# Kernel optimization log

Measured on AMD Instinct MI355X. Metric: run time of the kernel, lower is better.

The kernel has to match this reference:

```python
import jax, jax.numpy as jnp
import numpy as np

N, E, D_IN, D_H, D_OUT, W = 100000, 1600000, 128, 128, 128, 3
HTC_W, TEMP = 0.01, 1.0  # curvature c = 1.0


def _project(x):
    n = jnp.maximum(jnp.linalg.norm(x, axis=-1, keepdims=True), 1e-12)
    return x * jnp.minimum((1.0 - 1e-5) / n, 1.0)


def _artanh(x):
    x = jnp.clip(x, -1.0 + 1e-6, 1.0 - 1e-6)
    return 0.5 * (jnp.log1p(x) - jnp.log1p(-x))


def _expmap0(v):
    n = jnp.maximum(jnp.linalg.norm(v, axis=-1, keepdims=True), 1e-12)
    return _project(jnp.tanh(n) * v / n)


def _logmap0(y):
    y = _project(y)
    n = jnp.maximum(jnp.linalg.norm(y, axis=-1, keepdims=True), 1e-12)
    return _artanh(n) * y / n


def setup_inputs() -> dict:
    key = jax.random.key(0)
    ks = jax.random.split(key, 24)
    x = jax.random.normal(ks[0], (N, D_IN), dtype=jnp.float32)
    edge_index = jax.random.randint(ks[1], (2, E), 0, N)
    t = jax.random.uniform(ks[2], (E,), dtype=jnp.float32)
    prev_hyp = _project(jax.random.normal(ks[3], (N, D_OUT), dtype=jnp.float32) * 0.05)
    lengths = jax.random.randint(ks[4], (N,), 0, W + 1)
    valid_mask = jnp.arange(W)[None, :] < lengths[:, None]  # front-filled deque
    hist_hyp = _project(jax.random.normal(ks[5], (N, W, D_OUT), dtype=jnp.float32) * 0.05)
    hist_hyp = hist_hyp * valid_mask[..., None].astype(jnp.float32)  # padded slots are zero

    def lin(k, dout, din):
        return jax.random.normal(k, (dout, din), dtype=jnp.float32) / np.sqrt(din)

    params = dict(
        w_time=jax.random.normal(ks[6], (D_IN,), dtype=jnp.float32),
        b_time=jnp.zeros((D_IN,), jnp.float32),
        W0_l=lin(ks[7], D_H, D_IN), b0_l=jnp.zeros((D_H,), jnp.float32), W0_r=lin(ks[8], D_H, D_IN),
        W1_l=lin(ks[9], D_OUT, D_H), b1_l=jnp.zeros((D_OUT,), jnp.float32), W1_r=lin(ks[10], D_OUT, D_H),
        W_ih=lin(ks[11], 3 * D_OUT, D_OUT), W_hh=lin(ks[12], 3 * D_OUT, D_OUT),
        b_ih=jnp.zeros((3 * D_OUT,), jnp.float32), b_hh=jnp.zeros((3 * D_OUT,), jnp.float32),
        Wq=lin(ks[13], D_OUT, D_OUT), Wk=lin(ks[14], D_OUT, D_OUT), Wv=lin(ks[15], D_OUT, D_OUT),
    )
    return dict(x=x, edge_index=edge_index, t=t, prev_hyp=prev_hyp,
                hist_hyp=hist_hyp, valid_mask=valid_mask, **params)


def reference(x, edge_index, t, prev_hyp, hist_hyp, valid_mask,
              w_time, b_time, W0_l, b0_l, W0_r, W1_l, b1_l, W1_r,
              W_ih, W_hh, b_ih, b_hh, Wq, Wk, Wv):
    n = x.shape[0]
    src, dst = edge_index[0], edge_index[1]
    ones_e = jnp.ones_like(t)
    # per-node mean event time over incident edges (src and dst both count)
    nt = jax.ops.segment_sum(t, src, n) + jax.ops.segment_sum(t, dst, n)
    cnt = jax.ops.segment_sum(ones_e, src, n) + jax.ops.segment_sum(ones_e, dst, n)
    node_time = nt / jnp.maximum(cnt, 1.0)
    x = x + jnp.cos(node_time[:, None] * w_time[None, :] + b_time[None, :])
    # SAGEConv (mean aggr over incoming edges): out = W_l @ mean_j x_j + b + W_r @ x_i
    deg = jnp.maximum(jax.ops.segment_sum(ones_e, dst, n), 1.0)[:, None]
    agg0 = jax.ops.segment_sum(x[src], dst, n) / deg
    h = jax.nn.relu(agg0 @ W0_l.T + b0_l + x @ W0_r.T)
    agg1 = jax.ops.segment_sum(h[src], dst, n) / deg
    h_now = agg1 @ W1_l.T + b1_l + h @ W1_r.T  # tangent-space current embedding

    prev_tan = _logmap0(prev_hyp)
    # ragged history attention (padded + masked)
    hist_tan = _logmap0(hist_hyp)                       # [N, W, D]
    q = h_now @ Wq.T                                    # [N, D]
    k = hist_tan @ Wk.T                                 # [N, W, D]
    v = hist_tan @ Wv.T
    score = jnp.einsum('nwd,nd->nw', k, q) / (np.sqrt(D_OUT) * max(TEMP, 1e-6))
    has_hist = valid_mask.any(axis=-1, keepdims=True)
    score = jnp.where(valid_mask, score, -jnp.inf)
    score = jnp.where(has_hist, score, 0.0)
    alpha = jax.nn.softmax(score, axis=-1)
    alpha = jnp.where(has_hist, alpha, 0.0)
    ctx = jnp.einsum('nw,nwd->nd', alpha, v)

    # GRUCell(input=h_now, hidden=prev_tan + ctx)
    hidden = prev_tan + ctx
    gi = h_now @ W_ih.T + b_ih
    gh = hidden @ W_hh.T + b_hh
    i_r, i_z, i_n = jnp.split(gi, 3, axis=-1)
    h_r, h_z, h_n = jnp.split(gh, 3, axis=-1)
    r = jax.nn.sigmoid(i_r + h_r)
    z = jax.nn.sigmoid(i_z + h_z)
    nn_ = jnp.tanh(i_n + r * h_n)
    h_tan = (1.0 - z) * nn_ + z * hidden
    h_hyp = _expmap0(h_tan)

    # hyperbolic temporal consistency aux loss (c = 1)
    x_sq = jnp.sum(h_hyp * h_hyp, axis=-1)
    y_sq = jnp.sum(prev_hyp * prev_hyp, axis=-1)
    diff_sq = jnp.sum((h_hyp - prev_hyp) ** 2, axis=-1)
    denom = jnp.maximum((1.0 - x_sq) * (1.0 - y_sq), 1e-8)
    zarg = jnp.maximum(1.0 + 2.0 * diff_sq / denom, 1.0 + 1e-6)
    dist = jnp.arccosh(zarg)
    valid_prev = (jnp.sum(jnp.abs(prev_hyp), axis=-1) > 0).astype(dist.dtype)
    aux = HTC_W * jnp.sum(dist * valid_prev) / jnp.maximum(jnp.sum(valid_prev), 1.0)
    aux = jnp.where(jnp.any(valid_prev > 0), aux, 0.0)
    return h_hyp, aux
```

## Files before the change

kernel.cpp:

```cpp
#include <hip/hip_runtime.h>
#include <math.h>


typedef _Float16 f16x8 __attribute__((ext_vector_type(8)));
typedef _Float16 f16x4 __attribute__((ext_vector_type(4)));
typedef _Float16 f16x2 __attribute__((ext_vector_type(2)));
typedef float f32x4 __attribute__((ext_vector_type(4)));

__device__ __forceinline__ float wsum(float v) {
#pragma unroll
  for (int off = 1; off < 64; off <<= 1) v += __shfl_xor(v, off, 64);
  return v;
}

__device__ __forceinline__ void fsplit(float x, _Float16& h, _Float16& l) {
  h = (_Float16)x;
  l = (_Float16)(x - (float)h);
}

__device__ __forceinline__ float logmap_scale(float nrm2) {
  float n0 = fmaxf(sqrtf(nrm2), 1e-12f);
  float sp = fminf((1.0f - 1e-5f) / n0, 1.0f);
  float np = fmaxf(n0 * sp, 1e-12f);
  float a  = fminf(np, 1.0f - 1e-6f);
  float at = 0.5f * (log1pf(a) - log1pf(-a));
  return sp * at / np;
}

__global__ void k_edge(const int* __restrict__ ei, const float* __restrict__ t,
                       unsigned long long* __restrict__ packed, int E) {
  int e = blockIdx.x * 256 + threadIdx.x;
  if (e >= E) return;
  int s = ei[e], d = ei[E + e];
  unsigned long long tf =
      (unsigned long long)__float2uint_rn(t[e] * 16777216.0f);
  unsigned long long encs = tf | (1ULL << 40);
  atomicAdd(&packed[s], encs);
  atomicAdd(&packed[d], encs | (1ULL << 52));
}

__global__ void k_scan1(const unsigned long long* __restrict__ packed,
                        int* __restrict__ rowptr, int* __restrict__ bsum, int N) {
  __shared__ int s[256];
  int t = threadIdx.x;
  int base = blockIdx.x * 1024 + t * 4;
  int v[4]; int loc = 0;
#pragma unroll
  for (int j = 0; j < 4; ++j) {
    int i = base + j;
    v[j] = (i < N) ? (int)(packed[i] >> 52) : 0;
    loc += v[j];
  }
  s[t] = loc; __syncthreads();
  for (int off = 1; off < 256; off <<= 1) {
    int x = (t >= off) ? s[t - off] : 0; __syncthreads();
    s[t] += x; __syncthreads();
  }
  int run = s[t] - loc;
#pragma unroll
  for (int j = 0; j < 4; ++j) { int i = base + j; if (i < N) rowptr[i] = run; run += v[j]; }
  if (t == 255) bsum[blockIdx.x] = s[255];
}

__global__ void k_scan2(const int* __restrict__ bsum, int* __restrict__ boff, int nb) {
  __shared__ int s[128];
  int t = threadIdx.x;
  int v = (t < nb) ? bsum[t] : 0;
  s[t] = v; __syncthreads();
  for (int off = 1; off < 128; off <<= 1) {
    int x = (t >= off) ? s[t - off] : 0; __syncthreads();
    s[t] += x; __syncthreads();
  }
  boff[t] = s[t] - v;
}

__global__ void k_scan3(int* __restrict__ rowptr, const int* __restrict__ boff, int N, int E) {
  int i = blockIdx.x * 256 + threadIdx.x;
  if (i < N) rowptr[i] += boff[i >> 10];
  if (i == 0) rowptr[N] = E;
}

__global__ void k_scatter(const int* __restrict__ ei, const int* __restrict__ rowptr,
                          int* __restrict__ cursor, int* __restrict__ eidx, int E) {
  int e = blockIdx.x * 256 + threadIdx.x;
  if (e >= E) return;
  int s = ei[e], d = ei[E + e];
  int p = rowptr[d] + atomicAdd(&cursor[d], 1);
  eidx[p] = s;
}

__global__ void k_time(const float* __restrict__ x,
                       const unsigned long long* __restrict__ packed,
                       const float* __restrict__ wt,
                       const float* __restrict__ bt,
                       _Float16* __restrict__ out, int N) {
  int id = blockIdx.x * 256 + threadIdx.x;
  if (id >= N * 32) return;
  int n = id >> 5, q = id & 31;
  unsigned long long p = packed[n];
  float tsum = (float)(p & 0xFFFFFFFFFFULL) * 5.9604644775390625e-8f;
  int c = (int)((p >> 40) & 0xFFF);
  float tm = tsum / fmaxf((float)c, 1.0f);
  float4 xv = ((const float4*)x)[id];
  float4 wv = ((const float4*)wt)[q];
  float4 bv = ((const float4*)bt)[q];
  float o[4];
  o[0] = xv.x + cosf(tm * wv.x + bv.x);
  o[1] = xv.y + cosf(tm * wv.y + bv.y);
  o[2] = xv.z + cosf(tm * wv.z + bv.z);
  o[3] = xv.w + cosf(tm * wv.w + bv.w);
  f16x4 vh, vl;
#pragma unroll
  for (int j = 0; j < 4; ++j) { _Float16 h, l; fsplit(o[j], h, l); vh[j] = h; vl[j] = l; }
  *(f16x4*)&out[(size_t)n * 256 + q * 4] = vh;
  *(f16x4*)&out[(size_t)n * 256 + 128 + q * 4] = vl;
}

__global__ void k_agg(const _Float16* __restrict__ X, const int* __restrict__ rowptr,
                      const int* __restrict__ eidx, _Float16* __restrict__ out, int N) {
  int wid = threadIdx.x >> 6, lane = threadIdx.x & 63;
  int n = blockIdx.x * 4 + wid;
  if (n >= N) return;
  int s0 = rowptr[n], s1 = rowptr[n + 1];
  size_t lo4 = (size_t)lane * 4;
  float a0[4] = {0, 0, 0, 0}, a1[4] = {0, 0, 0, 0};
  float a2[4] = {0, 0, 0, 0}, a3[4] = {0, 0, 0, 0};
  int e = s0;
  for (; e + 4 <= s1; e += 4) {
    int i0 = eidx[e], i1 = eidx[e + 1], i2 = eidx[e + 2], i3 = eidx[e + 3];
    f16x4 v0 = *(const f16x4*)&X[(size_t)i0 * 256 + lo4];
    f16x4 v1 = *(const f16x4*)&X[(size_t)i1 * 256 + lo4];
    f16x4 v2 = *(const f16x4*)&X[(size_t)i2 * 256 + lo4];
    f16x4 v3 = *(const f16x4*)&X[(size_t)i3 * 256 + lo4];
#pragma unroll
    for (int j = 0; j < 4; ++j) {
      a0[j] += (float)v0[j]; a1[j] += (float)v1[j];
      a2[j] += (float)v2[j]; a3[j] += (float)v3[j];
    }
  }
  float a[4];
#pragma unroll
  for (int j = 0; j < 4; ++j) a[j] = (a0[j] + a1[j]) + (a2[j] + a3[j]);
  for (; e < s1; ++e) {
    int s = eidx[e];
    f16x4 v = *(const f16x4*)&X[(size_t)s * 256 + lo4];
#pragma unroll
    for (int j = 0; j < 4; ++j) a[j] += (float)v[j];
  }
  float lov[4];
#pragma unroll
  for (int j = 0; j < 4; ++j) lov[j] = __shfl(a[j], lane + 32, 64);
  if (lane < 32) {
    float sc = 1.0f / fmaxf((float)(s1 - s0), 1.0f);
    f16x4 vh, vl;
#pragma unroll
    for (int j = 0; j < 4; ++j) {
      float v = (a[j] + lov[j]) * sc;
      _Float16 h, l; fsplit(v, h, l);
      vh[j] = h; vl[j] = l;
    }
    *(f16x4*)&out[(size_t)n * 256 + lane * 4] = vh;
    *(f16x4*)&out[(size_t)n * 256 + 128 + lane * 4] = vl;
  }
}

__global__ void k_prep(const float* __restrict__ W0l, const float* __restrict__ W0r,
                       const float* __restrict__ W1l, const float* __restrict__ W1r,
                       const float* __restrict__ Wv,  const float* __restrict__ Wih,
                       const float* __restrict__ Whh, const float* __restrict__ bih,
                       const float* __restrict__ bhh,
                       _Float16* __restrict__ W0H, _Float16* __restrict__ W0L,
                       _Float16* __restrict__ W1H, _Float16* __restrict__ W1L,
                       _Float16* __restrict__ WvH, _Float16* __restrict__ WvL,
                       _Float16* __restrict__ WzH, _Float16* __restrict__ WzL,
                       float* __restrict__ bz) {
  int id = blockIdx.x * 256 + threadIdx.x;
  if (id < 32768) {
    int c = id >> 8, k = id & 255;
    float v0 = (k < 128) ? W0l[c * 128 + k] : W0r[c * 128 + (k - 128)];
    float v1 = (k < 128) ? W1l[c * 128 + k] : W1r[c * 128 + (k - 128)];
    fsplit(v0, W0H[id], W0L[id]);
    fsplit(v1, W1H[id], W1L[id]);
  }
  if (id < 16384) {
    fsplit(Wv[id], WvH[id], WvL[id]);
  }
  if (id < 131072) {
    int c = id >> 8, k = id & 255;
    float v;
    if (c < 256)      v = (k < 128) ? Wih[c * 128 + k] : Whh[c * 128 + (k - 128)];
    else if (c < 384) v = (k < 128) ? Wih[c * 128 + k] : 0.f;
    else              v = (k < 128) ? 0.f : Whh[(c - 128) * 128 + (k - 128)];
    fsplit(v, WzH[id], WzL[id]);
  }
  if (id < 512) {
    float v;
    if (id < 256)      v = bih[id] + bhh[id];
    else if (id < 384) v = bih[id];
    else               v = bhh[id - 128];
    bz[id] = v;
  }
}

__global__ void k_ct(const float* __restrict__ Wk, const float* __restrict__ Wq,
                     _Float16* __restrict__ CtH, _Float16* __restrict__ CtL) {
  int id = blockIdx.x * 256 + threadIdx.x;
  if (id >= 16384) return;
  int c = id >> 7, k = id & 127;
  float s = 0.f;
  for (int j = 0; j < 128; ++j) s += Wk[j * 128 + c] * Wq[j * 128 + k];
  fsplit(s, CtH[id], CtL[id]);
}

__global__ void k_lognorm(const float* __restrict__ Y, float* __restrict__ scale, int N) {
  int wid = threadIdx.x >> 6, lane = threadIdx.x & 63;
  int n = blockIdx.x * 4 + wid;
  if (n >= N) return;
  float2 y = ((const float2*)Y)[(size_t)n * 64 + lane];
  float nrm2 = wsum(y.x * y.x + y.y * y.y);
  if (lane == 0) scale[n] = logmap_scale(nrm2);
}

__global__ __launch_bounds__(256)
void k_mm(const _Float16* __restrict__ A1, const _Float16* __restrict__ A2,
          const _Float16* __restrict__ WH,  const _Float16* __restrict__ WL,
          const float* __restrict__ bias,   const float* __restrict__ addb,
          const float* __restrict__ scalev,
          float* __restrict__ outF, _Float16* __restrict__ outS,
          int Nrows, int Ktot, int Ctot, int relu) {
  __shared__ _Float16 sA[2][128][64];
  __shared__ _Float16 sW[2][128][64];
  const int tid = threadIdx.x;
  const int lane = tid & 63;
  const int wv = tid >> 6;
  const int wr = wv >> 1, wc = wv & 1;
  const int laneR = lane & 15, laneG = lane >> 4;
  const int n0 = blockIdx.x * 128;
  const int c0 = blockIdx.y * 128;

  f32x4 acc[4][4];
#pragma unroll
  for (int mi = 0; mi < 4; ++mi)
#pragma unroll
    for (int ni = 0; ni < 4; ++ni)
#pragma unroll
      for (int j = 0; j < 4; ++j) acc[mi][ni][j] = 0.f;

  const int nslab = Ktot >> 6;
  for (int s = 0; s < nslab; ++s) {
    int kglob = s << 6;
    const _Float16* Ax = (kglob < 128) ? A1 : A2;
    int kc = kglob & 127;
    __syncthreads();
#pragma unroll
    for (int it = 0; it < 4; ++it) {
      int idx = tid + (it << 8);
      int r = idx >> 3, chunk = idx & 7;
      int cs = (chunk ^ (r & 7)) << 3;
      int kq = chunk << 3;
      int n = n0 + r;
      f16x8 vh, vl;
      if (n < Nrows) {
        vh = *(const f16x8*)&Ax[(size_t)n * 256 + kc + kq];
        vl = *(const f16x8*)&Ax[(size_t)n * 256 + 128 + kc + kq];
      } else {
#pragma unroll
        for (int j = 0; j < 8; ++j) { vh[j] = (_Float16)0; vl[j] = (_Float16)0; }
      }
      *(f16x8*)&sA[0][r][cs] = vh;
      *(f16x8*)&sA[1][r][cs] = vl;
      int c = c0 + r;
      f16x8 wh = *(const f16x8*)&WH[(size_t)c * Ktot + kglob + kq];
      f16x8 wl = *(const f16x8*)&WL[(size_t)c * Ktot + kglob + kq];
      *(f16x8*)&sW[0][r][cs] = wh;
      *(f16x8*)&sW[1][r][cs] = wl;
    }
    __syncthreads();
#pragma unroll
    for (int kk = 0; kk < 2; ++kk) {
      f16x8 ah[4], al[4], bh[4], bl[4];
      int kch = (kk << 2) + laneG;
#pragma unroll
      for (int m = 0; m < 4; ++m) {
        int row = wr * 64 + m * 16 + laneR;
        int ko = (kch ^ (row & 7)) << 3;
        ah[m] = *(const f16x8*)&sA[0][row][ko];
        al[m] = *(const f16x8*)&sA[1][row][ko];
      }
#pragma unroll
      for (int n = 0; n < 4; ++n) {
        int row = wc * 64 + n * 16 + laneR;
        int ko = (kch ^ (row & 7)) << 3;
        bh[n] = *(const f16x8*)&sW[0][row][ko];
        bl[n] = *(const f16x8*)&sW[1][row][ko];
      }
#pragma unroll
      for (int m = 0; m < 4; ++m)
#pragma unroll
        for (int n = 0; n < 4; ++n) {
          acc[m][n] = __builtin_amdgcn_mfma_f32_16x16x32_f16(ah[m], bh[n], acc[m][n], 0, 0, 0);
          acc[m][n] = __builtin_amdgcn_mfma_f32_16x16x32_f16(al[m], bh[n], acc[m][n], 0, 0, 0);
          acc[m][n] = __builtin_amdgcn_mfma_f32_16x16x32_f16(ah[m], bl[n], acc[m][n], 0, 0, 0);
        }
    }
  }
#pragma unroll
  for (int m = 0; m < 4; ++m) {
#pragma unroll
    for (int n = 0; n < 4; ++n) {
      int rbase = n0 + wr * 64 + m * 16 + laneG * 4;
      int c = c0 + wc * 64 + n * 16 + laneR;
      float bval = bias ? bias[c] : 0.f;
#pragma unroll
      for (int j = 0; j < 4; ++j) {
        int r = rbase + j;
        if (r >= Nrows) continue;
        float v = acc[m][n][j] + bval;
        if (addb) {
          float ab = addb[(size_t)r * Ctot + c];
          v += scalev ? ab * scalev[r] : ab;
        }
        if (relu) v = fmaxf(v, 0.f);
        if (outF) outF[(size_t)r * Ctot + c] = v;
        if (outS) {
          _Float16 h, l; fsplit(v, h, l);
          outS[(size_t)r * 256 + c] = h;
          outS[(size_t)r * 256 + 128 + c] = l;
        }
      }
    }
  }
}

__global__ __launch_bounds__(256)
void k_mmu(const _Float16* __restrict__ A1, const _Float16* __restrict__ A2,
           const _Float16* __restrict__ WH, const _Float16* __restrict__ WL,
           const _Float16* __restrict__ CtH, const _Float16* __restrict__ CtL,
           const float* __restrict__ bias,
           _Float16* __restrict__ outS, float* __restrict__ outU, int Nrows) {
  __shared__ _Float16 sA[2][128][64];
  __shared__ _Float16 sW[2][128][64];
  const int tid = threadIdx.x;
  const int lane = tid & 63;
  const int wv = tid >> 6;
  const int wr = wv >> 1, wc = wv & 1;
  const int laneR = lane & 15, laneG = lane >> 4;
  const int n0 = blockIdx.x * 128;

  f32x4 acc[4][4];
#pragma unroll
  for (int mi = 0; mi < 4; ++mi)
#pragma unroll
    for (int ni = 0; ni < 4; ++ni)
#pragma unroll
      for (int j = 0; j < 4; ++j) acc[mi][ni][j] = 0.f;

  for (int s = 0; s < 4; ++s) {
    int kglob = s << 6;
    const _Float16* Ax = (kglob < 128) ? A1 : A2;
    int kc = kglob & 127;
    __syncthreads();
#pragma unroll
    for (int it = 0; it < 4; ++it) {
      int idx = tid + (it << 8);
      int r = idx >> 3, chunk = idx & 7;
      int cs = (chunk ^ (r & 7)) << 3;
      int kq = chunk << 3;
      int n = n0 + r;
      f16x8 vh, vl;
      if (n < Nrows) {
        vh = *(const f16x8*)&Ax[(size_t)n * 256 + kc + kq];
        vl = *(const f16x8*)&Ax[(size_t)n * 256 + 128 + kc + kq];
      } else {
#pragma unroll
        for (int j = 0; j < 8; ++j) { vh[j] = (_Float16)0; vl[j] = (_Float16)0; }
      }
      *(f16x8*)&sA[0][r][cs] = vh;
      *(f16x8*)&sA[1][r][cs] = vl;
      f16x8 wh = *(const f16x8*)&WH[(size_t)r * 256 + kglob + kq];
      f16x8 wl = *(const f16x8*)&WL[(size_t)r * 256 + kglob + kq];
      *(f16x8*)&sW[0][r][cs] = wh;
      *(f16x8*)&sW[1][r][cs] = wl;
    }
    __syncthreads();
#pragma unroll
    for (int kk = 0; kk < 2; ++kk) {
      f16x8 ah[4], al[4], bh[4], bl[4];
      int kch = (kk << 2) + laneG;
#pragma unroll
      for (int m = 0; m < 4; ++m) {
        int row = wr * 64 + m * 16 + laneR;
        int ko = (kch ^ (row & 7)) << 3;
        ah[m] = *(const f16x8*)&sA[0][row][ko];
        al[m] = *(const f16x8*)&sA[1][row][ko];
      }
#pragma unroll
      for (int n = 0; n < 4; ++n) {
        int row = wc * 64 + n * 16 + laneR;
        int ko = (kch ^ (row & 7)) << 3;
        bh[n] = *(const f16x8*)&sW[0][row][ko];
        bl[n] = *(const f16x8*)&sW[1][row][ko];
      }
#pragma unroll
      for (int m = 0; m < 4; ++m)
#pragma unroll
        for (int n = 0; n < 4; ++n) {
          acc[m][n] = __builtin_amdgcn_mfma_f32_16x16x32_f16(ah[m], bh[n], acc[m][n], 0, 0, 0);
          acc[m][n] = __builtin_amdgcn_mfma_f32_16x16x32_f16(al[m], bh[n], acc[m][n], 0, 0, 0);
          acc[m][n] = __builtin_amdgcn_mfma_f32_16x16x32_f16(ah[m], bl[n], acc[m][n], 0, 0, 0);
        }
    }
  }

  f32x4 accU[4][4];
#pragma unroll
  for (int mi = 0; mi < 4; ++mi)
#pragma unroll
    for (int ni = 0; ni < 4; ++ni)
#pragma unroll
      for (int j = 0; j < 4; ++j) accU[mi][ni][j] = 0.f;

  for (int us = 0; us < 2; ++us) {
    __syncthreads();
    if (wc == us) {
#pragma unroll
      for (int m = 0; m < 4; ++m)
#pragma unroll
        for (int n = 0; n < 4; ++n) {
          int kp = n * 16 + laneR;
          float bval = bias[us * 64 + n * 16 + laneR];
#pragma unroll
          for (int j = 0; j < 4; ++j) {
            int row = wr * 64 + m * 16 + laneG * 4 + j;
            float v = acc[m][n][j] + bval;
            _Float16 h, l; fsplit(v, h, l);
            int cs = ((kp >> 3) ^ (row & 7)) * 8 + (kp & 7);
            sA[0][row][cs] = h;
            sA[1][row][cs] = l;
          }
        }
    }
#pragma unroll
    for (int it = 0; it < 4; ++it) {
      int idx = tid + (it << 8);
      int r = idx >> 3, chunk = idx & 7;
      int cs = (chunk ^ (r & 7)) << 3;
      int kq = chunk << 3;
      *(f16x8*)&sW[0][r][cs] = *(const f16x8*)&CtH[(size_t)r * 128 + us * 64 + kq];
      *(f16x8*)&sW[1][r][cs] = *(const f16x8*)&CtL[(size_t)r * 128 + us * 64 + kq];
    }
    __syncthreads();
#pragma unroll
    for (int kk = 0; kk < 2; ++kk) {
      f16x8 ah[4], al[4], bh[4], bl[4];
      int kch = (kk << 2) + laneG;
#pragma unroll
      for (int m = 0; m < 4; ++m) {
        int row = wr * 64 + m * 16 + laneR;
        int ko = (kch ^ (row & 7)) << 3;
        ah[m] = *(const f16x8*)&sA[0][row][ko];
        al[m] = *(const f16x8*)&sA[1][row][ko];
      }
#pragma unroll
      for (int n = 0; n < 4; ++n) {
        int row = wc * 64 + n * 16 + laneR;
        int ko = (kch ^ (row & 7)) << 3;
        bh[n] = *(const f16x8*)&sW[0][row][ko];
        bl[n] = *(const f16x8*)&sW[1][row][ko];
      }
#pragma unroll
      for (int m = 0; m < 4; ++m)
#pragma unroll
        for (int n = 0; n < 4; ++n) {
          accU[m][n] = __builtin_amdgcn_mfma_f32_16x16x32_f16(ah[m], bh[n], accU[m][n], 0, 0, 0);
          accU[m][n] = __builtin_amdgcn_mfma_f32_16x16x32_f16(al[m], bh[n], accU[m][n], 0, 0, 0);
          accU[m][n] = __builtin_amdgcn_mfma_f32_16x16x32_f16(ah[m], bl[n], accU[m][n], 0, 0, 0);
        }
    }
  }

#pragma unroll
  for (int m = 0; m < 4; ++m) {
#pragma unroll
    for (int n = 0; n < 4; ++n) {
      int rbase = n0 + wr * 64 + m * 16 + laneG * 4;
      int c = wc * 64 + n * 16 + laneR;
      float bval = bias[c];
#pragma unroll
      for (int j = 0; j < 4; ++j) {
        int r = rbase + j;
        if (r >= Nrows) continue;
        float v = acc[m][n][j] + bval;
        _Float16 h, l; fsplit(v, h, l);
        outS[(size_t)r * 256 + c] = h;
        outS[(size_t)r * 256 + 128 + c] = l;
        outU[(size_t)r * 128 + c] = accU[m][n][j];
      }
    }
  }
}

__global__ void k_attn(const float* __restrict__ U, const float* __restrict__ hist,
                       _Float16* __restrict__ out, int N) {
  int wid = threadIdx.x >> 6, lane = threadIdx.x & 63;
  int n = blockIdx.x * 4 + wid;
  if (n >= N) return;
  float2 u = ((const float2*)U)[(size_t)n * 64 + lane];
  float htx[3], hty[3], sc[3];
  bool val[3];
#pragma unroll
  for (int w = 0; w < 3; ++w) {
    float2 h = ((const float2*)hist)[((size_t)n * 3 + w) * 64 + lane];
    float nrm2 = wsum(h.x * h.x + h.y * h.y);
    val[w] = nrm2 > 0.f;
    float s = logmap_scale(nrm2);
    htx[w] = h.x * s; hty[w] = h.y * s;
    float d = wsum(htx[w] * u.x + hty[w] * u.y);
    sc[w] = d * 0.0883883476483184f;
  }
  float cx = 0.f, cy = 0.f;
  if (val[0] || val[1] || val[2]) {
    float m = -INFINITY;
#pragma unroll
    for (int w = 0; w < 3; ++w) if (val[w]) m = fmaxf(m, sc[w]);
    float a[3]; float ssum = 0.f;
#pragma unroll
    for (int w = 0; w < 3; ++w) { a[w] = val[w] ? expf(sc[w] - m) : 0.f; ssum += a[w]; }
    float inv = 1.f / ssum;
#pragma unroll
    for (int w = 0; w < 3; ++w) { cx += htx[w] * (a[w] * inv); cy += hty[w] * (a[w] * inv); }
  }
  _Float16 hx, lx, hy, ly;
  fsplit(cx, hx, lx); fsplit(cy, hy, ly);
  f16x2 vh = {hx, hy}, vl = {lx, ly};
  *(f16x2*)&out[(size_t)n * 256 + lane * 2] = vh;
  *(f16x2*)&out[(size_t)n * 256 + 128 + lane * 2] = vl;
}

__global__ __launch_bounds__(256, 2)
void k_gru(const _Float16* __restrict__ P0c, const _Float16* __restrict__ P2c,
           const _Float16* __restrict__ WzH, const _Float16* __restrict__ WzL,
           const float* __restrict__ bz, const float* __restrict__ prev,
           float* __restrict__ out, float* __restrict__ pd,
           float* __restrict__ pv, int N) {
  __shared__ _Float16 sA[2][64][64];
  __shared__ _Float16 sW[2][128][64];
  __shared__ float rn1[64][2];
  __shared__ float rn3[64][2][3];
  __shared__ float distrow[64], validrow[64];
  const int tid = threadIdx.x;
  const int lane = tid & 63;
  const int wv = tid >> 6;
  const int wr = wv >> 1, wc = wv & 1;
  const int laneR = lane & 15, laneG = lane >> 4;
  const int n0 = blockIdx.x * 64;

  f32x4 acc[4][2][4];
#pragma unroll
  for (int q = 0; q < 4; ++q)
#pragma unroll
    for (int m = 0; m < 2; ++m)
#pragma unroll
      for (int n = 0; n < 4; ++n)
#pragma unroll
        for (int j = 0; j < 4; ++j) acc[q][m][n][j] = 0.f;

#define STAGE_W(Q)                                                          \
  {                                                                         \
    _Pragma("unroll")                                                       \
    for (int it = 0; it < 4; ++it) {                                        \
      int idx = tid + (it << 8);                                            \
      int r = idx >> 3, chunk = idx & 7;                                    \
      int cs = (chunk ^ (r & 7)) << 3;                                      \
      int kq = chunk << 3;                                                  \
      size_t wrow = (size_t)((Q)*128 + r);                                  \
      *(f16x8*)&sW[0][r][cs] = *(const f16x8*)&WzH[wrow * 256 + kglob + kq];\
      *(f16x8*)&sW[1][r][cs] = *(const f16x8*)&WzL[wrow * 256 + kglob + kq];\
    }                                                                       \
  }

#define COMPUTE_Q(Q)                                                        \
  {                                                                         \
    _Pragma("unroll")                                                       \
    for (int kk = 0; kk < 2; ++kk) {                                        \
      int kch = (kk << 2) + laneG;                                          \
      f16x8 ah[2], al[2], bh[4], bl[4];                                     \
      _Pragma("unroll")                                                     \
      for (int m = 0; m < 2; ++m) {                                         \
        int row = wr * 32 + m * 16 + laneR;                                 \
        int ko = (kch ^ (row & 7)) << 3;                                    \
        ah[m] = *(const f16x8*)&sA[0][row][ko];                             \
        al[m] = *(const f16x8*)&sA[1][row][ko];                             \
      }                                                                     \
      _Pragma("unroll")                                                     \
      for (int n = 0; n < 4; ++n) {                                         \
        int row = wc * 64 + n * 16 + laneR;                                 \
        int ko = (kch ^ (row & 7)) << 3;                                    \
        bh[n] = *(const f16x8*)&sW[0][row][ko];                             \
        bl[n] = *(const f16x8*)&sW[1][row][ko];                             \
      }                                                                     \
      _Pragma("unroll")                                                     \
      for (int m = 0; m < 2; ++m)                                           \
        _Pragma("unroll")                                                   \
        for (int n = 0; n < 4; ++n) {                                       \
          acc[Q][m][n] = __builtin_amdgcn_mfma_f32_16x16x32_f16(ah[m], bh[n], acc[Q][m][n], 0, 0, 0); \
          acc[Q][m][n] = __builtin_amdgcn_mfma_f32_16x16x32_f16(al[m], bh[n], acc[Q][m][n], 0, 0, 0); \
          acc[Q][m][n] = __builtin_amdgcn_mfma_f32_16x16x32_f16(ah[m], bl[n], acc[Q][m][n], 0, 0, 0); \
        }                                                                   \
    }                                                                       \
  }

#pragma unroll
  for (int s = 0; s < 4; ++s) {
    int kglob = s << 6;
    const _Float16* Ax = (s < 2) ? P0c : P2c;
    int kc = kglob & 127;
    __syncthreads();
#pragma unroll
    for (int it = 0; it < 2; ++it) {
      int idx = tid + (it << 8);
      int r = idx >> 3, chunk = idx & 7;
      int cs = (chunk ^ (r & 7)) << 3;
      int kq = chunk << 3;
      int n = n0 + r;
      f16x8 vh, vl;
      if (n < N) {
        vh = *(const f16x8*)&Ax[(size_t)n * 256 + kc + kq];
        vl = *(const f16x8*)&Ax[(size_t)n * 256 + 128 + kc + kq];
      } else {
#pragma unroll
        for (int j = 0; j < 8; ++j) { vh[j] = (_Float16)0; vl[j] = (_Float16)0; }
      }
      *(f16x8*)&sA[0][r][cs] = vh;
      *(f16x8*)&sA[1][r][cs] = vl;
    }
    STAGE_W(0);
    __syncthreads();
    COMPUTE_Q(0);
    __syncthreads();
    STAGE_W(1);
    __syncthreads();
    COMPUTE_Q(1);
    __syncthreads();
    if (s < 2) {
      STAGE_W(2);
      __syncthreads();
      COMPUTE_Q(2);
    } else {
      STAGE_W(3);
      __syncthreads();
      COMPUTE_Q(3);
    }
  }
#undef STAGE_W
#undef COMPUTE_Q

  float bz0[4], bz1[4], bz2[4], bz3[4];
#pragma unroll
  for (int n = 0; n < 4; ++n) {
    int d = wc * 64 + n * 16 + laneR;
    bz0[n] = bz[d]; bz1[n] = bz[128 + d]; bz2[n] = bz[256 + d]; bz3[n] = bz[384 + d];
  }
  float tv[2][4][4];
#pragma unroll
  for (int m = 0; m < 2; ++m)
#pragma unroll
    for (int n = 0; n < 4; ++n)
#pragma unroll
      for (int j = 0; j < 4; ++j) {
        int row = n0 + wr * 32 + m * 16 + laneG * 4 + j;
        int d = wc * 64 + n * 16 + laneR;
        float hid = 0.f;
        if (row < N) {
          size_t o = (size_t)row * 256 + d;
          hid = (float)P2c[o] + (float)P2c[o + 128];
        }
        float gr = acc[0][m][n][j] + bz0[n];
        float gz = acc[1][m][n][j] + bz1[n];
        float gi = acc[2][m][n][j] + bz2[n];
        float gh = acc[3][m][n][j] + bz3[n];
        float rr = 1.f / (1.f + expf(-gr));
        float zz = 1.f / (1.f + expf(-gz));
        float nn = tanhf(gi + rr * gh);
        tv[m][n][j] = (1.f - zz) * nn + zz * hid;
      }
#pragma unroll
  for (int m = 0; m < 2; ++m)
#pragma unroll
    for (int j = 0; j < 4; ++j) {
      float p = 0.f;
#pragma unroll
      for (int n = 0; n < 4; ++n) p += tv[m][n][j] * tv[m][n][j];
#pragma unroll
      for (int off = 1; off < 16; off <<= 1) p += __shfl_xor(p, off, 64);
      if (laneR == 0) rn1[wr * 32 + m * 16 + laneG * 4 + j][wc] = p;
    }
  __syncthreads();
  float hv[2][4][4];
#pragma unroll
  for (int m = 0; m < 2; ++m)
#pragma unroll
    for (int j = 0; j < 4; ++j) {
      int rl = wr * 32 + m * 16 + laneG * 4 + j;
      int row = n0 + rl;
      float nv2 = rn1[rl][0] + rn1[rl][1];
      float nv = fmaxf(sqrtf(nv2), 1e-12f);
      float tn = tanhf(nv);
      float s1 = tn / nv;
      float nw = fmaxf(tn, 1e-12f);
      float sp = fminf((1.f - 1e-5f) / nw, 1.f);
      float scl = s1 * sp;
#pragma unroll
      for (int n = 0; n < 4; ++n) {
        float h = tv[m][n][j] * scl;
        hv[m][n][j] = h;
        int d = wc * 64 + n * 16 + laneR;
        if (row < N) out[(size_t)row * 128 + d] = h;
      }
    }
#pragma unroll
  for (int m = 0; m < 2; ++m)
#pragma unroll
    for (int j = 0; j < 4; ++j) {
      int rl = wr * 32 + m * 16 + laneG * 4 + j;
      int row = n0 + rl;
      float ys = 0.f, ds = 0.f, pa = 0.f;
#pragma unroll
      for (int n = 0; n < 4; ++n) {
        int d = wc * 64 + n * 16 + laneR;
        float p = (row < N) ? prev[(size_t)row * 128 + d] : 0.f;
        float h = hv[m][n][j];
        ys += p * p; ds += (h - p) * (h - p); pa += fabsf(p);
      }
#pragma unroll
      for (int off = 1; off < 16; off <<= 1) {
        ys += __shfl_xor(ys, off, 64);
        ds += __shfl_xor(ds, off, 64);
        pa += __shfl_xor(pa, off, 64);
      }
      if (laneR == 0) { rn3[rl][wc][0] = ys; rn3[rl][wc][1] = ds; rn3[rl][wc][2] = pa; }
    }
  __syncthreads();
  if (wc == 0 && laneR == 0) {
#pragma unroll
    for (int m = 0; m < 2; ++m)
#pragma unroll
      for (int j = 0; j < 4; ++j) {
        int rl = wr * 32 + m * 16 + laneG * 4 + j;
        int row = n0 + rl;
        float nv2 = rn1[rl][0] + rn1[rl][1];
        float nv = fmaxf(sqrtf(nv2), 1e-12f);
        float tn = tanhf(nv);
        float s1 = tn / nv;
        float nw = fmaxf(tn, 1e-12f);
        float sp = fminf((1.f - 1e-5f) / nw, 1.f);
        float scl = s1 * sp;
        float x_sq = scl * scl * nv2;
        float y_sq = rn3[rl][0][0] + rn3[rl][1][0];
        float d_sq = rn3[rl][0][1] + rn3[rl][1][1];
        float pab  = rn3[rl][0][2] + rn3[rl][1][2];
        float denom = fmaxf((1.f - x_sq) * (1.f - y_sq), 1e-8f);
        float zarg = fmaxf(1.f + 2.f * d_sq / denom, 1.f + 1e-6f);
        float dist = acoshf(zarg);
        float valid = (pab > 0.f && row < N) ? 1.f : 0.f;
        distrow[rl] = dist * valid;
        validrow[rl] = valid;
      }
  }
  __syncthreads();
  if (tid < 64) {
    float dv = distrow[tid], vvv = validrow[tid];
    dv = wsum(dv); vvv = wsum(vvv);
    if (tid == 0) { pd[blockIdx.x] = dv; pv[blockIdx.x] = vvv; }
  }
}

__global__ void k_reduce(const float* __restrict__ pd, const float* __restrict__ pv,
                         float* __restrict__ aux_out, int nparts) {
  __shared__ float sd[256], sv[256];
  float a = 0.f, b = 0.f;
  for (int i = threadIdx.x; i < nparts; i += 256) { a += pd[i]; b += pv[i]; }
  sd[threadIdx.x] = a; sv[threadIdx.x] = b; __syncthreads();
  for (int off = 128; off > 0; off >>= 1) {
    if (threadIdx.x < off) { sd[threadIdx.x] += sd[threadIdx.x + off]; sv[threadIdx.x] += sv[threadIdx.x + off]; }
    __syncthreads();
  }
  if (threadIdx.x == 0) {
    float aux = (sv[0] > 0.f) ? 0.01f * sd[0] / fmaxf(sv[0], 1.f) : 0.f;
    aux_out[0] = aux;
  }
}

extern "C" void kernel_launch(void* const* d_in, const int* in_sizes, int n_in,
                              void* d_out, int out_size, void* d_ws, size_t ws_size,
                              hipStream_t stream) {
  const float* x      = (const float*)d_in[0];
  const int*   ei     = (const int*)  d_in[1];
  const float* t      = (const float*)d_in[2];
  const float* prev   = (const float*)d_in[3];
  const float* hist   = (const float*)d_in[4];
  const float* w_time = (const float*)d_in[6];
  const float* b_time = (const float*)d_in[7];
  const float* W0l    = (const float*)d_in[8];
  const float* b0l    = (const float*)d_in[9];
  const float* W0r    = (const float*)d_in[10];
  const float* W1l    = (const float*)d_in[11];
  const float* b1l    = (const float*)d_in[12];
  const float* W1r    = (const float*)d_in[13];
  const float* Wih    = (const float*)d_in[14];
  const float* Whh    = (const float*)d_in[15];
  const float* bih    = (const float*)d_in[16];
  const float* bhh    = (const float*)d_in[17];
  const float* Wq     = (const float*)d_in[18];
  const float* Wk     = (const float*)d_in[19];
  const float* Wv     = (const float*)d_in[20];

  const int N = in_sizes[0] / 128;
  const int E = in_sizes[1] / 2;
  const int NB4 = (N + 3) / 4;
  const int NB1 = (N + 1023) / 1024;
  const int NBG = (N + 63) / 64;

  char* wbase = (char*)d_ws;
  size_t off = 0;
  auto alloc = [&](size_t bytes) -> void* {
    off = (off + 255) & ~(size_t)255;
    void* p = wbase + off; off += bytes; return p;
  };
  unsigned long long* packed = (unsigned long long*)alloc((size_t)N * 8);
  int*   cursor = (int*)  alloc((size_t)N * 4);
  size_t zero_bytes = off;
  int*   rowptr = (int*)  alloc((size_t)(N + 1) * 4);
  int*   bsum   = (int*)  alloc(512);
  int*   boff   = (int*)  alloc(512);
  int*   eidx   = (int*)  alloc((size_t)E * 4);
  _Float16* W0H = (_Float16*)alloc(32768 * 2);
  _Float16* W0L = (_Float16*)alloc(32768 * 2);
  _Float16* W1H = (_Float16*)alloc(32768 * 2);
  _Float16* W1L = (_Float16*)alloc(32768 * 2);
  _Float16* CtH = (_Float16*)alloc(16384 * 2);
  _Float16* CtL = (_Float16*)alloc(16384 * 2);
  _Float16* WvH = (_Float16*)alloc(16384 * 2);
  _Float16* WvL = (_Float16*)alloc(16384 * 2);
  _Float16* WzH = (_Float16*)alloc(131072 * 2);
  _Float16* WzL = (_Float16*)alloc(131072 * 2);
  float* bz     = (float*)alloc(512 * 4);
  float* scale  = (float*)alloc((size_t)N * 4);
  float* F0     = (float*)alloc((size_t)N * 128 * 4);
  _Float16* P0c = (_Float16*)alloc((size_t)N * 256 * 2);
  _Float16* P1c = (_Float16*)alloc((size_t)N * 256 * 2);
  _Float16* P2c = (_Float16*)alloc((size_t)N * 256 * 2);
  float* pd = (float*)alloc((size_t)NBG * 4);
  float* pv = (float*)alloc((size_t)NBG * 4);
  (void)ws_size; (void)n_in; (void)out_size;

  float* out_h   = (float*)d_out;
  float* out_aux = out_h + (size_t)N * 128;

  hipMemsetAsync(d_ws, 0, zero_bytes, stream);

  k_prep<<<512, 256, 0, stream>>>(W0l, W0r, W1l, W1r, Wv, Wih, Whh, bih, bhh,
                                  W0H, W0L, W1H, W1L, WvH, WvL, WzH, WzL, bz);
  k_ct<<<64, 256, 0, stream>>>(Wk, Wq, CtH, CtL);
  k_lognorm<<<NB4, 256, 0, stream>>>(prev, scale, N);

  int ebl = (E + 255) / 256;
  k_edge<<<ebl, 256, 0, stream>>>(ei, t, packed, E);
  k_scan1<<<NB1, 256, 0, stream>>>(packed, rowptr, bsum, N);
  k_scan2<<<1, 128, 0, stream>>>(bsum, boff, NB1);
  k_scan3<<<(N + 255) / 256, 256, 0, stream>>>(rowptr, boff, N, E);
  k_scatter<<<ebl, 256, 0, stream>>>(ei, rowptr, cursor, eidx, E);

  k_time<<<(N * 32 + 255) / 256, 256, 0, stream>>>(x, packed, w_time, b_time,
                                                   P0c, N);
  k_agg<<<NB4, 256, 0, stream>>>(P0c, rowptr, eidx, P1c, N);
  dim3 gb((N + 127) / 128, 1);
  k_mm<<<gb, 256, 0, stream>>>(P1c, P0c, W0H, W0L, b0l, nullptr, nullptr,
                               nullptr, P2c, N, 256, 128, 1);
  k_agg<<<NB4, 256, 0, stream>>>(P2c, rowptr, eidx, P1c, N);
  k_mmu<<<gb, 256, 0, stream>>>(P1c, P2c, W1H, W1L, CtH, CtL, b1l, P0c, F0, N);
  k_attn<<<NB4, 256, 0, stream>>>(F0, hist, P1c, N);
  k_mm<<<gb, 256, 0, stream>>>(P1c, nullptr, WvH, WvL, nullptr, prev, scale,
                               nullptr, P2c, N, 128, 128, 0);
  k_gru<<<NBG, 256, 0, stream>>>(P0c, P2c, WzH, WzL, bz, prev,
                                 out_h, pd, pv, N);
  k_reduce<<<1, 256, 0, stream>>>(pd, pv, out_aux, NBG);
}
```

Measured before the change: 1.122 ms.

## Merge independent prep kernels and load GEMM tiles directly into LDS

Independent setup kernels (edge atomics, weight splitting, Ct product, log-norm scale) are merged into one launch through block-range dispatch, and scatter is merged with the time-encoding kernel, cutting launch count and letting the pieces overlap. The GEMM tile loads in k_mm and k_mmu switch from global-to-register-to-LDS copies to global_load_lds direct transfers with a per-lane XOR-swizzled source address. Out-of-range rows are clamped to the last valid row instead of being zero-filled, which is only safe if those rows are never written back. The direct-to-LDS layout relies on the wave-contiguous write order matching the swizzled read pattern.

```diff
diff --git a/kernel.cpp b/kernel.cpp
--- a/kernel.cpp
+++ b/kernel.cpp
@@ -16,6 +16,12 @@
 __device__ __forceinline__ void fsplit(float x, _Float16& h, _Float16& l) {
   h = (_Float16)x;
   l = (_Float16)(x - (float)h);
+}
+
+typedef const __attribute__((address_space(1))) unsigned int* gas_ptr;
+typedef __attribute__((address_space(3))) unsigned int* las_ptr;
+__device__ __forceinline__ void gld16(const void* g, void* l) {
+  __builtin_amdgcn_global_load_lds((gas_ptr)g, (las_ptr)l, 16, 0, 0);
 }
 
 __device__ __forceinline__ float logmap_scale(float nrm2) {
@@ -27,16 +33,82 @@
   return sp * at / np;
 }
 
-__global__ void k_edge(const int* __restrict__ ei, const float* __restrict__ t,
-                       unsigned long long* __restrict__ packed, int E) {
-  int e = blockIdx.x * 256 + threadIdx.x;
-  if (e >= E) return;
-  int s = ei[e], d = ei[E + e];
-  unsigned long long tf =
-      (unsigned long long)__float2uint_rn(t[e] * 16777216.0f);
-  unsigned long long encs = tf | (1ULL << 40);
-  atomicAdd(&packed[s], encs);
-  atomicAdd(&packed[d], encs | (1ULL << 52));
+__global__ void k_edgeprep(const int* __restrict__ ei, const float* __restrict__ t,
+                           unsigned long long* __restrict__ packed, int E, int ebl,
+                           const float* __restrict__ Wk, const float* __restrict__ Wq,
+                           _Float16* __restrict__ CtH, _Float16* __restrict__ CtL,
+                           const float* __restrict__ prevY, float* __restrict__ scale,
+                           int N, int NB4,
+                           const float* __restrict__ W0l, const float* __restrict__ W0r,
+                           const float* __restrict__ W1l, const float* __restrict__ W1r,
+                           const float* __restrict__ Wv,  const float* __restrict__ Wih,
+                           const float* __restrict__ Whh, const float* __restrict__ bih,
+                           const float* __restrict__ bhh,
+                           _Float16* __restrict__ W0H, _Float16* __restrict__ W0L,
+                           _Float16* __restrict__ W1H, _Float16* __restrict__ W1L,
+                           _Float16* __restrict__ WvH, _Float16* __restrict__ WvL,
+                           _Float16* __restrict__ WzH, _Float16* __restrict__ WzL,
+                           float* __restrict__ bz) {
+  int bid = blockIdx.x;
+  if (bid < ebl) {
+    int e = bid * 256 + threadIdx.x;
+    if (e >= E) return;
+    int s = ei[e], d = ei[E + e];
+    unsigned long long tf =
+        (unsigned long long)__float2uint_rn(t[e] * 16777216.0f);
+    unsigned long long encs = tf | (1ULL << 40);
+    atomicAdd(&packed[s], encs);
+    atomicAdd(&packed[d], encs | (1ULL << 52));
+    return;
+  }
+  bid -= ebl;
+  if (bid < 64) {
+    int id = bid * 256 + threadIdx.x;
+    int c = id >> 7, k = id & 127;
+    float s = 0.f;
+    for (int j = 0; j < 128; ++j) s += Wk[j * 128 + c] * Wq[j * 128 + k];
+    fsplit(s, CtH[id], CtL[id]);
+    return;
+  }
+  bid -= 64;
+  if (bid < NB4) {
+    int wid = threadIdx.x >> 6, lane = threadIdx.x & 63;
+    int n = bid * 4 + wid;
+    if (n >= N) return;
+    float2 y = ((const float2*)prevY)[(size_t)n * 64 + lane];
+    float nrm2 = wsum(y.x * y.x + y.y * y.y);
+    if (lane == 0) scale[n] = logmap_scale(nrm2);
+    return;
+  }
+  bid -= NB4;
+  {
+    int id = bid * 256 + threadIdx.x;
+    if (id < 32768) {
+      int c = id >> 8, k = id & 255;
+      float v0 = (k < 128) ? W0l[c * 128 + k] : W0r[c * 128 + (k - 128)];
+      float v1 = (k < 128) ? W1l[c * 128 + k] : W1r[c * 128 + (k - 128)];
+      fsplit(v0, W0H[id], W0L[id]);
+      fsplit(v1, W1H[id], W1L[id]);
+    }
+    if (id < 16384) {
+      fsplit(Wv[id], WvH[id], WvL[id]);
+    }
+    if (id < 131072) {
+      int c = id >> 8, k = id & 255;
+      float v;
+      if (c < 256)      v = (k < 128) ? Wih[c * 128 + k] : Whh[c * 128 + (k - 128)];
+      else if (c < 384) v = (k < 128) ? Wih[c * 128 + k] : 0.f;
+      else              v = (k < 128) ? 0.f : Whh[(c - 128) * 128 + (k - 128)];
+      fsplit(v, WzH[id], WzL[id]);
+    }
+    if (id < 512) {
+      float v;
+      if (id < 256)      v = bih[id] + bhh[id];
+      else if (id < 384) v = bih[id];
+      else               v = bhh[id - 128];
+      bz[id] = v;
+    }
+  }
 }
 
 __global__ void k_scan1(const unsigned long long* __restrict__ packed,
@@ -80,40 +152,45 @@
   if (i == 0) rowptr[N] = E;
 }
 
-__global__ void k_scatter(const int* __restrict__ ei, const int* __restrict__ rowptr,
-                          int* __restrict__ cursor, int* __restrict__ eidx, int E) {
-  int e = blockIdx.x * 256 + threadIdx.x;
-  if (e >= E) return;
-  int s = ei[e], d = ei[E + e];
-  int p = rowptr[d] + atomicAdd(&cursor[d], 1);
-  eidx[p] = s;
-}
-
-__global__ void k_time(const float* __restrict__ x,
-                       const unsigned long long* __restrict__ packed,
-                       const float* __restrict__ wt,
-                       const float* __restrict__ bt,
-                       _Float16* __restrict__ out, int N) {
-  int id = blockIdx.x * 256 + threadIdx.x;
-  if (id >= N * 32) return;
-  int n = id >> 5, q = id & 31;
-  unsigned long long p = packed[n];
-  float tsum = (float)(p & 0xFFFFFFFFFFULL) * 5.9604644775390625e-8f;
-  int c = (int)((p >> 40) & 0xFFF);
-  float tm = tsum / fmaxf((float)c, 1.0f);
-  float4 xv = ((const float4*)x)[id];
-  float4 wv = ((const float4*)wt)[q];
-  float4 bv = ((const float4*)bt)[q];
-  float o[4];
-  o[0] = xv.x + cosf(tm * wv.x + bv.x);
-  o[1] = xv.y + cosf(tm * wv.y + bv.y);
-  o[2] = xv.z + cosf(tm * wv.z + bv.z);
-  o[3] = xv.w + cosf(tm * wv.w + bv.w);
-  f16x4 vh, vl;
-#pragma unroll
-  for (int j = 0; j < 4; ++j) { _Float16 h, l; fsplit(o[j], h, l); vh[j] = h; vl[j] = l; }
-  *(f16x4*)&out[(size_t)n * 256 + q * 4] = vh;
-  *(f16x4*)&out[(size_t)n * 256 + 128 + q * 4] = vl;
+__global__ void k_scattime(const int* __restrict__ ei, const int* __restrict__ rowptr,
+                           int* __restrict__ cursor, int* __restrict__ eidx, int E,
+                           int ebl,
+                           const float* __restrict__ x,
+                           const unsigned long long* __restrict__ packed,
+                           const float* __restrict__ wt, const float* __restrict__ bt,
+                           _Float16* __restrict__ out, int N) {
+  int bid = blockIdx.x;
+  if (bid < ebl) {
+    int e = bid * 256 + threadIdx.x;
+    if (e >= E) return;
+    int s = ei[e], d = ei[E + e];
+    int p = rowptr[d] + atomicAdd(&cursor[d], 1);
+    eidx[p] = s;
+    return;
+  }
+  bid -= ebl;
+  {
+    int id = bid * 256 + threadIdx.x;
+    if (id >= N * 32) return;
+    int n = id >> 5, q = id & 31;
+    unsigned long long p = packed[n];
+    float tsum = (float)(p & 0xFFFFFFFFFFULL) * 5.9604644775390625e-8f;
+    int c = (int)((p >> 40) & 0xFFF);
+    float tm = tsum / fmaxf((float)c, 1.0f);
+    float4 xv = ((const float4*)x)[id];
+    float4 wv = ((const float4*)wt)[q];
+    float4 bv = ((const float4*)bt)[q];
+    float o[4];
+    o[0] = xv.x + cosf(tm * wv.x + bv.x);
+    o[1] = xv.y + cosf(tm * wv.y + bv.y);
+    o[2] = xv.z + cosf(tm * wv.z + bv.z);
+    o[3] = xv.w + cosf(tm * wv.w + bv.w);
+    f16x4 vh, vl;
+#pragma unroll
+    for (int j = 0; j < 4; ++j) { _Float16 h, l; fsplit(o[j], h, l); vh[j] = h; vl[j] = l; }
+    *(f16x4*)&out[(size_t)n * 256 + q * 4] = vh;
+    *(f16x4*)&out[(size_t)n * 256 + 128 + q * 4] = vl;
+  }
 }
 
 __global__ void k_agg(const _Float16* __restrict__ X, const int* __restrict__ rowptr,
@@ -164,63 +241,6 @@
   }
 }
 
-__global__ void k_prep(const float* __restrict__ W0l, const float* __restrict__ W0r,
-                       const float* __restrict__ W1l, const float* __restrict__ W1r,
-                       const float* __restrict__ Wv,  const float* __restrict__ Wih,
-                       const float* __restrict__ Whh, const float* __restrict__ bih,
-                       const float* __restrict__ bhh,
-                       _Float16* __restrict__ W0H, _Float16* __restrict__ W0L,
-                       _Float16* __restrict__ W1H, _Float16* __restrict__ W1L,
-                       _Float16* __restrict__ WvH, _Float16* __restrict__ WvL,
-                       _Float16* __restrict__ WzH, _Float16* __restrict__ WzL,
-                       float* __restrict__ bz) {
-  int id = blockIdx.x * 256 + threadIdx.x;
-  if (id < 32768) {
-    int c = id >> 8, k = id & 255;
-    float v0 = (k < 128) ? W0l[c * 128 + k] : W0r[c * 128 + (k - 128)];
-    float v1 = (k < 128) ? W1l[c * 128 + k] : W1r[c * 128 + (k - 128)];
-    fsplit(v0, W0H[id], W0L[id]);
-    fsplit(v1, W1H[id], W1L[id]);
-  }
-  if (id < 16384) {
-    fsplit(Wv[id], WvH[id], WvL[id]);
-  }
-  if (id < 131072) {
-    int c = id >> 8, k = id & 255;
-    float v;
-    if (c < 256)      v = (k < 128) ? Wih[c * 128 + k] : Whh[c * 128 + (k - 128)];
-    else if (c < 384) v = (k < 128) ? Wih[c * 128 + k] : 0.f;
-    else              v = (k < 128) ? 0.f : Whh[(c - 128) * 128 + (k - 128)];
-    fsplit(v, WzH[id], WzL[id]);
-  }
-  if (id < 512) {
-    float v;
-    if (id < 256)      v = bih[id] + bhh[id];
-    else if (id < 384) v = bih[id];
-    else               v = bhh[id - 128];
-    bz[id] = v;
-  }
-}
-
-__global__ void k_ct(const float* __restrict__ Wk, const float* __restrict__ Wq,
-                     _Float16* __restrict__ CtH, _Float16* __restrict__ CtL) {
-  int id = blockIdx.x * 256 + threadIdx.x;
-  if (id >= 16384) return;
-  int c = id >> 7, k = id & 127;
-  float s = 0.f;
-  for (int j = 0; j < 128; ++j) s += Wk[j * 128 + c] * Wq[j * 128 + k];
-  fsplit(s, CtH[id], CtL[id]);
-}
-
-__global__ void k_lognorm(const float* __restrict__ Y, float* __restrict__ scale, int N) {
-  int wid = threadIdx.x >> 6, lane = threadIdx.x & 63;
-  int n = blockIdx.x * 4 + wid;
-  if (n >= N) return;
-  float2 y = ((const float2*)Y)[(size_t)n * 64 + lane];
-  float nrm2 = wsum(y.x * y.x + y.y * y.y);
-  if (lane == 0) scale[n] = logmap_scale(nrm2);
-}
-
 __global__ __launch_bounds__(256)
 void k_mm(const _Float16* __restrict__ A1, const _Float16* __restrict__ A2,
           const _Float16* __restrict__ WH,  const _Float16* __restrict__ WL,
@@ -253,27 +273,16 @@
     int kc = kglob & 127;
     __syncthreads();
 #pragma unroll
-    for (int it = 0; it < 4; ++it) {
-      int idx = tid + (it << 8);
-      int r = idx >> 3, chunk = idx & 7;
-      int cs = (chunk ^ (r & 7)) << 3;
-      int kq = chunk << 3;
-      int n = n0 + r;
-      f16x8 vh, vl;
-      if (n < Nrows) {
-        vh = *(const f16x8*)&Ax[(size_t)n * 256 + kc + kq];
-        vl = *(const f16x8*)&Ax[(size_t)n * 256 + 128 + kc + kq];
-      } else {
-#pragma unroll
-        for (int j = 0; j < 8; ++j) { vh[j] = (_Float16)0; vl[j] = (_Float16)0; }
-      }
-      *(f16x8*)&sA[0][r][cs] = vh;
-      *(f16x8*)&sA[1][r][cs] = vl;
-      int c = c0 + r;
-      f16x8 wh = *(const f16x8*)&WH[(size_t)c * Ktot + kglob + kq];
-      f16x8 wl = *(const f16x8*)&WL[(size_t)c * Ktot + kglob + kq];
-      *(f16x8*)&sW[0][r][cs] = wh;
-      *(f16x8*)&sW[1][r][cs] = wl;
+    for (int j = 0; j < 4; ++j) {
+      int rbase = (wv * 4 + j) * 8;
+      int row = rbase + (lane >> 3);
+      int sc = ((lane & 7) ^ (row & 7)) << 3;
+      int nA = n0 + row; if (nA >= Nrows) nA = Nrows - 1;
+      gld16(&Ax[(size_t)nA * 256 + kc + sc],       &sA[0][rbase][0]);
+      gld16(&Ax[(size_t)nA * 256 + 128 + kc + sc], &sA[1][rbase][0]);
+      int cW = c0 + row;
+      gld16(&WH[(size_t)cW * Ktot + kglob + sc],   &sW[0][rbase][0]);
+      gld16(&WL[(size_t)cW * Ktot + kglob + sc],   &sW[1][rbase][0]);
     }
     __syncthreads();
 #pragma unroll
@@ -361,26 +370,15 @@
     int kc = kglob & 127;
     __syncthreads();
 #pragma unroll
-    for (int it = 0; it < 4; ++it) {
-      int idx = tid + (it << 8);
-      int r = idx >> 3, chunk = idx & 7;
-      int cs = (chunk ^ (r & 7)) << 3;
-      int kq = chunk << 3;
-      int n = n0 + r;
-      f16x8 vh, vl;
-      if (n < Nrows) {
-        vh = *(const f16x8*)&Ax[(size_t)n * 256 + kc + kq];
-        vl = *(const f16x8*)&Ax[(size_t)n * 256 + 128 + kc + kq];
-      } else {
-#pragma unroll
-        for (int j = 0; j < 8; ++j) { vh[j] = (_Float16)0; vl[j] = (_Float16)0; }
-      }
-      *(f16x8*)&sA[0][r][cs] = vh;
-      *(f16x8*)&sA[1][r][cs] = vl;
-      f16x8 wh = *(const f16x8*)&WH[(size_t)r * 256 + kglob + kq];
-      f16x8 wl = *(const f16x8*)&WL[(size_t)r * 256 + kglob + kq];
-      *(f16x8*)&sW[0][r][cs] = wh;
-      *(f16x8*)&sW[1][r][cs] = wl;
+    for (int j = 0; j < 4; ++j) {
+      int rbase = (wv * 4 + j) * 8;
+      int row = rbase + (lane >> 3);
+      int sc = ((lane & 7) ^ (row & 7)) << 3;
+      int nA = n0 + row; if (nA >= Nrows) nA = Nrows - 1;
+      gld16(&Ax[(size_t)nA * 256 + kc + sc],       &sA[0][rbase][0]);
+      gld16(&Ax[(size_t)nA * 256 + 128 + kc + sc], &sA[1][rbase][0]);
+      gld16(&WH[(size_t)row * 256 + kglob + sc],   &sW[0][rbase][0]);
+      gld16(&WL[(size_t)row * 256 + kglob + sc],   &sW[1][rbase][0]);
     }
     __syncthreads();
 #pragma unroll
@@ -441,13 +439,12 @@
         }
     }
 #pragma unroll
-    for (int it = 0; it < 4; ++it) {
-      int idx = tid + (it << 8);
-      int r = idx >> 3, chunk = idx & 7;
-      int cs = (chunk ^ (r & 7)) << 3;
-      int kq = chunk << 3;
-      *(f16x8*)&sW[0][r][cs] = *(const f16x8*)&CtH[(size_t)r * 128 + us * 64 + kq];
-      *(f16x8*)&sW[1][r][cs] = *(const f16x8*)&CtL[(size_t)r * 128 + us * 64 + kq];
+    for (int j = 0; j < 4; ++j) {
+      int rbase = (wv * 4 + j) * 8;
+      int row = rbase + (lane >> 3);
+      int sc = ((lane & 7) ^ (row & 7)) << 3;
+      gld16(&CtH[(size_t)row * 128 + us * 64 + sc], &sW[0][rbase][0]);
+      gld16(&CtL[(size_t)row * 128 + us * 64 + sc], &sW[1][rbase][0]);
     }
     __syncthreads();
 #pragma unroll
@@ -859,20 +856,17 @@
 
   hipMemsetAsync(d_ws, 0, zero_bytes, stream);
 
-  k_prep<<<512, 256, 0, stream>>>(W0l, W0r, W1l, W1r, Wv, Wih, Whh, bih, bhh,
-                                  W0H, W0L, W1H, W1L, WvH, WvL, WzH, WzL, bz);
-  k_ct<<<64, 256, 0, stream>>>(Wk, Wq, CtH, CtL);
-  k_lognorm<<<NB4, 256, 0, stream>>>(prev, scale, N);
-
   int ebl = (E + 255) / 256;
-  k_edge<<<ebl, 256, 0, stream>>>(ei, t, packed, E);
+  k_edgeprep<<<ebl + 64 + NB4 + 512, 256, 0, stream>>>(
+      ei, t, packed, E, ebl, Wk, Wq, CtH, CtL, prev, scale, N, NB4,
+      W0l, W0r, W1l, W1r, Wv, Wih, Whh, bih, bhh,
+      W0H, W0L, W1H, W1L, WvH, WvL, WzH, WzL, bz);
   k_scan1<<<NB1, 256, 0, stream>>>(packed, rowptr, bsum, N);
   k_scan2<<<1, 128, 0, stream>>>(bsum, boff, NB1);
   k_scan3<<<(N + 255) / 256, 256, 0, stream>>>(rowptr, boff, N, E);
-  k_scatter<<<ebl, 256, 0, stream>>>(ei, rowptr, cursor, eidx, E);
-
-  k_time<<<(N * 32 + 255) / 256, 256, 0, stream>>>(x, packed, w_time, b_time,
-                                                   P0c, N);
+  k_scattime<<<ebl + (N * 32 + 255) / 256, 256, 0, stream>>>(
+      ei, rowptr, cursor, eidx, E, ebl, x, packed, w_time, b_time, P0c, N);
+
   k_agg<<<NB4, 256, 0, stream>>>(P0c, rowptr, eidx, P1c, N);
   dim3 gb((N + 127) / 128, 1);
   k_mm<<<gb, 256, 0, stream>>>(P1c, P0c, W0H, W0L, b0l, nullptr, nullptr,
```

New measurement: 1.140 ms. Within noise of the previous version (+1.6%).
